# Kernel tuning notes

Hardware: AMD Instinct MI355X
Metric: run time of the kernel (lower is better)

## Reference

```python
import jax, jax.numpy as jnp
import numpy as np

B, T, D_IN, H, NH, R = 32, 1024, 64, 128, 4, 3
HD = H // NH  # 32


def _p(key, shape, scale=0.02):
    return jax.random.normal(key, shape, dtype=jnp.float32) * scale


def setup_inputs() -> dict:
    key = jax.random.key(0)
    ks = jax.random.split(key, 8)
    return {
        "x": jax.random.normal(ks[0], (B, T, D_IN), dtype=jnp.float32),
        "theta_w": _p(ks[1], (H, D_IN)),
        "theta_b": jnp.zeros((H,), jnp.float32),
        "in_proj_w": _p(ks[2], (3 * H, H)),
        "in_proj_b": jnp.zeros((3 * H,), jnp.float32),
        "out_proj_w": _p(ks[3], (H, H)),
        "out_proj_b": jnp.zeros((H,), jnp.float32),
        "ln_g": jnp.ones((H,), jnp.float32),
        "ln_b": jnp.zeros((H,), jnp.float32),
        "w1": _p(ks[4], (H, H)),
        "b1": jnp.zeros((H,), jnp.float32),
        "w2": _p(ks[5], (2, H)),
        "b2": jnp.zeros((2,), jnp.float32),
    }


def _build_adj(t, radius):
    # banded adjacency: adj[i,j] = 1/(1+|i-j|) for |i-j| <= radius, row-normalized
    idx = jnp.arange(t)
    d = jnp.abs(idx[:, None] - idx[None, :])
    adj = jnp.where(d <= radius, 1.0 / (1.0 + d.astype(jnp.float32)), 0.0)
    return adj / jnp.clip(adj.sum(axis=1, keepdims=True), 1e-8)


def reference(x, theta_w, theta_b, in_proj_w, in_proj_b, out_proj_w, out_proj_b,
              ln_g, ln_b, w1, b1, w2, b2):
    h = x @ theta_w.T + theta_b                       # [B,T,H]
    adj = _build_adj(T, R)                            # [T,T]
    g = jnp.einsum('ij,bjh->bih', adj, h)             # banded temporal aggregation

    # torch nn.MultiheadAttention (batch_first, eval -> no dropout)
    qkv = g @ in_proj_w.T + in_proj_b                 # [B,T,3H]
    q, k, v = jnp.split(qkv, 3, axis=-1)
    split_heads = lambda t: t.reshape(B, T, NH, HD).transpose(0, 2, 1, 3)
    q, k, v = split_heads(q), split_heads(k), split_heads(v)
    scores = jnp.einsum('bntd,bnsd->bnts', q, k) / jnp.sqrt(jnp.float32(HD))
    attn = jax.nn.softmax(scores, axis=-1)
    o = jnp.einsum('bnts,bnsd->bntd', attn, v)
    o = o.transpose(0, 2, 1, 3).reshape(B, T, H)
    a = o @ out_proj_w.T + out_proj_b                 # [B,T,H]

    # head on last timestep: LayerNorm -> Linear -> GELU(exact) -> Linear
    last = a[:, -1, :]                                # [B,H]
    mu = last.mean(-1, keepdims=True)
    var = ((last - mu) ** 2).mean(-1, keepdims=True)
    ln = (last - mu) / jnp.sqrt(var + 1e-5) * ln_g + ln_b
    hid = jax.nn.gelu(ln @ w1.T + b1, approximate=False)
    return hid @ w2.T + b2                            # [B,2]
```

## Files before the change

### kernel.cpp

```cpp
#include <hip/hip_runtime.h>
#include <math.h>

#define TT 1024

__global__ __launch_bounds__(256) void k_qr(
    const float* __restrict__ x, const float* __restrict__ theta_w,
    const float* __restrict__ theta_b, const float* __restrict__ ipw,
    const float* __restrict__ ipb, float* __restrict__ r_out) {
  const int b = blockIdx.x;
  const int tid = threadIdx.x;
  __shared__ float s_xs[64];
  __shared__ float s_y[128];
  __shared__ float s_q[128];
  __shared__ float s_z[4][128];
  const float* __restrict__ xb = x + (size_t)b * TT * 64;

  if (tid < 64) {
    float acc = xb[(TT - 1) * 64 + tid]
              + 0.5f        * xb[(TT - 2) * 64 + tid]
              + (1.f / 3.f) * xb[(TT - 3) * 64 + tid]
              + 0.25f       * xb[(TT - 4) * 64 + tid];
    s_xs[tid] = acc * (12.f / 25.f);
  }
  __syncthreads();
  if (tid < 128) {
    const float* tr = theta_w + tid * 64;
    float acc = theta_b[tid];
    for (int d = 0; d < 64; ++d) acc += tr[d] * s_xs[d];
    s_y[tid] = acc;
  }
  __syncthreads();
  {
    const int g = tid >> 4, l = tid & 15;
    for (int pass = 0; pass < 8; ++pass) {
      const int e = pass * 16 + g;
      const float* wr = ipw + e * 128 + l * 8;
      float acc = 0.f;
      #pragma unroll
      for (int u = 0; u < 8; ++u) acc += wr[u] * s_y[l * 8 + u];
      acc += __shfl_xor(acc, 1);
      acc += __shfl_xor(acc, 2);
      acc += __shfl_xor(acc, 4);
      acc += __shfl_xor(acc, 8);
      if (l == 0) s_q[e] = acc + ipb[e];
    }
  }
  __syncthreads();
  for (int rep = 0; rep < 2; ++rep) {
    const int idx = tid + rep * 256;
    const int n = idx >> 7, c = idx & 127;
    const float* qn = &s_q[n * 32];
    float acc = 0.f;
    for (int e = 0; e < 32; ++e) acc += ipw[(128 + n * 32 + e) * 128 + c] * qn[e];
    s_z[n][c] = acc;
  }
  __syncthreads();
  {
    const int n = tid >> 6, d = tid & 63;
    const float* zn = s_z[n];
    float acc = 0.f;
    for (int c = 0; c < 128; ++c) acc += theta_w[c * 64 + d] * zn[c];
    r_out[(b * 4 + n) * 64 + d] = acc * 0.17677669529663687f;
  }
}

__global__ __launch_bounds__(256) void k_t(
    const float* __restrict__ x, const float* __restrict__ r_in,
    float* __restrict__ t_out) {
  const int b = blockIdx.x >> 4;
  const int chunk = blockIdx.x & 15;
  const int tid = threadIdx.x;
  __shared__ __align__(16) float s_r[256];
  s_r[tid] = r_in[b * 256 + tid];
  __syncthreads();
  const int g = tid >> 4, l = tid & 15;
  const float4 r0 = ((const float4*)(s_r +   0))[l];
  const float4 r1 = ((const float4*)(s_r +  64))[l];
  const float4 r2 = ((const float4*)(s_r + 128))[l];
  const float4 r3 = ((const float4*)(s_r + 192))[l];
  const float* __restrict__ xb = x + ((size_t)b * TT + chunk * 64) * 64;
  for (int it = 0; it < 4; ++it) {
    const int jj = it * 16 + g;
    const float4 xv = ((const float4*)(xb + jj * 64))[l];
    float p0 = xv.x * r0.x + xv.y * r0.y + xv.z * r0.z + xv.w * r0.w;
    float p1 = xv.x * r1.x + xv.y * r1.y + xv.z * r1.z + xv.w * r1.w;
    float p2 = xv.x * r2.x + xv.y * r2.y + xv.z * r2.z + xv.w * r2.w;
    float p3 = xv.x * r3.x + xv.y * r3.y + xv.z * r3.z + xv.w * r3.w;
    #pragma unroll
    for (int m = 1; m <= 8; m <<= 1) {
      p0 += __shfl_xor(p0, m);
      p1 += __shfl_xor(p1, m);
      p2 += __shfl_xor(p2, m);
      p3 += __shfl_xor(p3, m);
    }
    if (l == 0) {
      const int j = chunk * 64 + jj;
      t_out[(b * 4 + 0) * TT + j] = p0;
      t_out[(b * 4 + 1) * TT + j] = p1;
      t_out[(b * 4 + 2) * TT + j] = p2;
      t_out[(b * 4 + 3) * TT + j] = p3;
    }
  }
}

__global__ __launch_bounds__(256) void k_sm(float* __restrict__ t_pt) {
  const int bn = blockIdx.x;
  const int tid = threadIdx.x;
  __shared__ __align__(16) float s_t[TT];
  __shared__ float s_p[TT];
  __shared__ float s_red[4];
  ((float4*)s_t)[tid] = ((const float4*)(t_pt + bn * TT))[tid];
  __syncthreads();

  float sc[4], wsv[4];
  float lmax = -1e30f;
  const int s0 = tid * 4;
  for (int k = 0; k < 4; ++k) {
    const int s = s0 + k;
    float acc = 0.f, wsum = 0.f;
    #pragma unroll
    for (int dj = -3; dj <= 3; ++dj) {
      const int j = s + dj;
      if (j >= 0 && j < TT) {
        const float w = 1.f / (1.f + (float)(dj < 0 ? -dj : dj));
        acc += w * s_t[j];
        wsum += w;
      }
    }
    sc[k] = acc / wsum;
    wsv[k] = wsum;
    lmax = fmaxf(lmax, sc[k]);
  }
  #pragma unroll
  for (int m = 32; m >= 1; m >>= 1) lmax = fmaxf(lmax, __shfl_xor(lmax, m));
  if ((tid & 63) == 0) s_red[tid >> 6] = lmax;
  __syncthreads();
  const float bmax = fmaxf(fmaxf(s_red[0], s_red[1]), fmaxf(s_red[2], s_red[3]));
  __syncthreads();
  float lsum = 0.f;
  for (int k = 0; k < 4; ++k) {
    const float e = expf(sc[k] - bmax);
    lsum += e;
    s_p[s0 + k] = e / wsv[k];
  }
  #pragma unroll
  for (int m = 32; m >= 1; m >>= 1) lsum += __shfl_xor(lsum, m);
  if ((tid & 63) == 0) s_red[tid >> 6] = lsum;
  __syncthreads();
  const float inv_denom = 1.f / (s_red[0] + s_red[1] + s_red[2] + s_red[3]);
  for (int k = 0; k < 4; ++k) {
    const int j = s0 + k;
    float acc = 0.f;
    #pragma unroll
    for (int dj = -3; dj <= 3; ++dj) {
      const int s = j + dj;
      if (s >= 0 && s < TT)
        acc += (1.f / (1.f + (float)(dj < 0 ? -dj : dj))) * s_p[s];
    }
    t_pt[bn * TT + j] = acc * inv_denom;
  }
}

__global__ __launch_bounds__(256) void k_u(
    const float* __restrict__ x, const float* __restrict__ pt_in,
    float* __restrict__ up_out) {
  const int b = blockIdx.x >> 4;
  const int chunk = blockIdx.x & 15;
  const int tid = threadIdx.x;
  __shared__ __align__(16) float s_x[64][64];
  __shared__ float s_p[4][64];
  const float* __restrict__ xb = x + ((size_t)b * TT + chunk * 64) * 64;
  #pragma unroll
  for (int it = 0; it < 4; ++it) {
    const int i4 = tid + it * 256;
    ((float4*)&s_x[0][0])[i4] = ((const float4*)xb)[i4];
  }
  {
    const int n = tid >> 6, jj = tid & 63;
    s_p[n][jj] = pt_in[(b * 4 + n) * TT + chunk * 64 + jj];
  }
  __syncthreads();
  const int n = tid >> 6, d = tid & 63;
  float acc = 0.f;
  for (int jj = 0; jj < 64; ++jj) acc += s_p[n][jj] * s_x[jj][d];
  up_out[((b * 16 + chunk) * 4 + n) * 64 + d] = acc;
}

__global__ __launch_bounds__(128) void k_tail(
    const float* __restrict__ up_in, const float* __restrict__ theta_w,
    const float* __restrict__ theta_b, const float* __restrict__ ipw,
    const float* __restrict__ ipb, const float* __restrict__ Wout,
    const float* __restrict__ outb, const float* __restrict__ ln_g,
    const float* __restrict__ ln_b, const float* __restrict__ w1,
    const float* __restrict__ b1, const float* __restrict__ w2,
    const float* __restrict__ b2, float* __restrict__ out) {
  const int b = blockIdx.x;
  const int tid = threadIdx.x;
  __shared__ float s_u[256];
  __shared__ float s_w[4][128];
  __shared__ float s_o[128], s_ln[128], s_hid[128], s_red[2];

  for (int rep = 0; rep < 2; ++rep) {
    const int idx = tid + rep * 128;
    float acc = 0.f;
    for (int c = 0; c < 16; ++c) acc += up_in[(b * 16 + c) * 256 + idx];
    s_u[idx] = acc;
  }
  __syncthreads();
  for (int rep = 0; rep < 4; ++rep) {
    const int idx = tid + rep * 128;
    const int n = idx >> 7, c = idx & 127;
    const float* tr = theta_w + c * 64;
    const float* un = &s_u[n * 64];
    float acc = theta_b[c];
    for (int d = 0; d < 64; ++d) acc += tr[d] * un[d];
    s_w[n][c] = acc;
  }
  __syncthreads();
  {
    const int e = tid, n = e >> 5;
    const float* wr = ipw + (256 + e) * 128;
    const float* wn = s_w[n];
    float acc = ipb[256 + e];
    for (int c = 0; c < 128; ++c) acc += wr[c] * wn[c];
    s_o[e] = acc;
  }
  __syncthreads();
  const int e = tid;
  float a = outb[e];
  {
    const float* wr = Wout + e * 128;
    for (int f = 0; f < 128; ++f) a += wr[f] * s_o[f];
  }
  float sum = a;
  #pragma unroll
  for (int m = 32; m >= 1; m >>= 1) sum += __shfl_xor(sum, m);
  if ((e & 63) == 0) s_red[e >> 6] = sum;
  __syncthreads();
  const float mu = (s_red[0] + s_red[1]) * (1.f / 128.f);
  __syncthreads();
  const float d = a - mu;
  float sq = d * d;
  #pragma unroll
  for (int m = 32; m >= 1; m >>= 1) sq += __shfl_xor(sq, m);
  if ((e & 63) == 0) s_red[e >> 6] = sq;
  __syncthreads();
  const float var = (s_red[0] + s_red[1]) * (1.f / 128.f);
  const float ln = d / sqrtf(var + 1e-5f) * ln_g[e] + ln_b[e];
  s_ln[e] = ln;
  __syncthreads();
  float h = b1[e];
  {
    const float* w1r = w1 + e * 128;
    for (int f = 0; f < 128; ++f) h += w1r[f] * s_ln[f];
  }
  h = 0.5f * h * (1.f + erff(h * 0.70710678118654752f));
  s_hid[e] = h;
  __syncthreads();
  if (e < 2) {
    float acc = b2[e];
    const float* w2r = w2 + e * 128;
    for (int f = 0; f < 128; ++f) acc += w2r[f] * s_hid[f];
    out[b * 2 + e] = acc;
  }
}

extern "C" void kernel_launch(void* const* d_in, const int* in_sizes, int n_in,
                              void* d_out, int out_size, void* d_ws, size_t ws_size,
                              hipStream_t stream) {
  const float* x       = (const float*)d_in[0];
  const float* theta_w = (const float*)d_in[1];
  const float* theta_b = (const float*)d_in[2];
  const float* ipw     = (const float*)d_in[3];
  const float* ipb     = (const float*)d_in[4];
  const float* outw    = (const float*)d_in[5];
  const float* outb    = (const float*)d_in[6];
  const float* ln_g    = (const float*)d_in[7];
  const float* ln_b    = (const float*)d_in[8];
  const float* w1      = (const float*)d_in[9];
  const float* b1      = (const float*)d_in[10];
  const float* w2      = (const float*)d_in[11];
  const float* b2      = (const float*)d_in[12];

  float* ws = (float*)d_ws;
  float* r  = ws;
  float* t  = ws + 8192;
  float* up = ws + 8192 + 131072;

  k_qr  <<< 32, 256, 0, stream>>>(x, theta_w, theta_b, ipw, ipb, r);
  k_t   <<<512, 256, 0, stream>>>(x, r, t);
  k_sm  <<<128, 256, 0, stream>>>(t);
  k_u   <<<512, 256, 0, stream>>>(x, t, up);
  k_tail<<< 32, 128, 0, stream>>>(up, theta_w, theta_b, ipw, ipb, outw, outb,
                                  ln_g, ln_b, w1, b1, w2, b2, (float*)d_out);
}
```

Before: 118.0 us.

## Fuse score, softmax, aggregation and head into one kernel via last-block counter

```diff
diff --git a/kernel.cpp b/kernel.cpp
--- a/kernel.cpp
+++ b/kernel.cpp
@@ -2,11 +2,13 @@
 #include <math.h>
 
 #define TT 1024
+
 
 __global__ __launch_bounds__(256) void k_qr(
     const float* __restrict__ x, const float* __restrict__ theta_w,
     const float* __restrict__ theta_b, const float* __restrict__ ipw,
-    const float* __restrict__ ipb, float* __restrict__ r_out) {
+    const float* __restrict__ ipb, float* __restrict__ r_out,
+    int* __restrict__ cnt) {
   const int b = blockIdx.x;
   const int tid = threadIdx.x;
   __shared__ float s_xs[64];
@@ -15,6 +17,8 @@
   __shared__ float s_z[4][128];
   const float* __restrict__ xb = x + (size_t)b * TT * 64;
 
+  if (tid == 0) cnt[b] = 0;
+
   if (tid < 64) {
     float acc = xb[(TT - 1) * 64 + tid]
               + 0.5f        * xb[(TT - 2) * 64 + tid]
@@ -64,204 +68,210 @@
   }
 }
 
-__global__ __launch_bounds__(256) void k_t(
+__global__ __launch_bounds__(256) void k_main(
     const float* __restrict__ x, const float* __restrict__ r_in,
-    float* __restrict__ t_out) {
+    float* __restrict__ t_ws, int* __restrict__ cnt,
+    const float* __restrict__ theta_w, const float* __restrict__ theta_b,
+    const float* __restrict__ ipw, const float* __restrict__ ipb,
+    const float* __restrict__ Wout, const float* __restrict__ outb,
+    const float* __restrict__ ln_g, const float* __restrict__ ln_b,
+    const float* __restrict__ w1, const float* __restrict__ b1,
+    const float* __restrict__ w2, const float* __restrict__ b2,
+    float* __restrict__ out) {
   const int b = blockIdx.x >> 4;
   const int chunk = blockIdx.x & 15;
   const int tid = threadIdx.x;
+
   __shared__ __align__(16) float s_r[256];
-  s_r[tid] = r_in[b * 256 + tid];
-  __syncthreads();
-  const int g = tid >> 4, l = tid & 15;
-  const float4 r0 = ((const float4*)(s_r +   0))[l];
-  const float4 r1 = ((const float4*)(s_r +  64))[l];
-  const float4 r2 = ((const float4*)(s_r + 128))[l];
-  const float4 r3 = ((const float4*)(s_r + 192))[l];
-  const float* __restrict__ xb = x + ((size_t)b * TT + chunk * 64) * 64;
-  for (int it = 0; it < 4; ++it) {
-    const int jj = it * 16 + g;
-    const float4 xv = ((const float4*)(xb + jj * 64))[l];
-    float p0 = xv.x * r0.x + xv.y * r0.y + xv.z * r0.z + xv.w * r0.w;
-    float p1 = xv.x * r1.x + xv.y * r1.y + xv.z * r1.z + xv.w * r1.w;
-    float p2 = xv.x * r2.x + xv.y * r2.y + xv.z * r2.z + xv.w * r2.w;
-    float p3 = xv.x * r3.x + xv.y * r3.y + xv.z * r3.z + xv.w * r3.w;
-    #pragma unroll
-    for (int m = 1; m <= 8; m <<= 1) {
-      p0 += __shfl_xor(p0, m);
-      p1 += __shfl_xor(p1, m);
-      p2 += __shfl_xor(p2, m);
-      p3 += __shfl_xor(p3, m);
-    }
-    if (l == 0) {
-      const int j = chunk * 64 + jj;
-      t_out[(b * 4 + 0) * TT + j] = p0;
-      t_out[(b * 4 + 1) * TT + j] = p1;
-      t_out[(b * 4 + 2) * TT + j] = p2;
-      t_out[(b * 4 + 3) * TT + j] = p3;
-    }
-  }
-}
-
-__global__ __launch_bounds__(256) void k_sm(float* __restrict__ t_pt) {
-  const int bn = blockIdx.x;
-  const int tid = threadIdx.x;
-  __shared__ __align__(16) float s_t[TT];
-  __shared__ float s_p[TT];
-  __shared__ float s_red[4];
-  ((float4*)s_t)[tid] = ((const float4*)(t_pt + bn * TT))[tid];
-  __syncthreads();
-
-  float sc[4], wsv[4];
-  float lmax = -1e30f;
-  const int s0 = tid * 4;
-  for (int k = 0; k < 4; ++k) {
-    const int s = s0 + k;
-    float acc = 0.f, wsum = 0.f;
-    #pragma unroll
-    for (int dj = -3; dj <= 3; ++dj) {
-      const int j = s + dj;
-      if (j >= 0 && j < TT) {
-        const float w = 1.f / (1.f + (float)(dj < 0 ? -dj : dj));
-        acc += w * s_t[j];
-        wsum += w;
-      }
-    }
-    sc[k] = acc / wsum;
-    wsv[k] = wsum;
-    lmax = fmaxf(lmax, sc[k]);
-  }
-  #pragma unroll
-  for (int m = 32; m >= 1; m >>= 1) lmax = fmaxf(lmax, __shfl_xor(lmax, m));
-  if ((tid & 63) == 0) s_red[tid >> 6] = lmax;
-  __syncthreads();
-  const float bmax = fmaxf(fmaxf(s_red[0], s_red[1]), fmaxf(s_red[2], s_red[3]));
-  __syncthreads();
-  float lsum = 0.f;
-  for (int k = 0; k < 4; ++k) {
-    const float e = expf(sc[k] - bmax);
-    lsum += e;
-    s_p[s0 + k] = e / wsv[k];
-  }
-  #pragma unroll
-  for (int m = 32; m >= 1; m >>= 1) lsum += __shfl_xor(lsum, m);
-  if ((tid & 63) == 0) s_red[tid >> 6] = lsum;
-  __syncthreads();
-  const float inv_denom = 1.f / (s_red[0] + s_red[1] + s_red[2] + s_red[3]);
-  for (int k = 0; k < 4; ++k) {
-    const int j = s0 + k;
-    float acc = 0.f;
-    #pragma unroll
-    for (int dj = -3; dj <= 3; ++dj) {
-      const int s = j + dj;
-      if (s >= 0 && s < TT)
-        acc += (1.f / (1.f + (float)(dj < 0 ? -dj : dj))) * s_p[s];
-    }
-    t_pt[bn * TT + j] = acc * inv_denom;
-  }
-}
-
-__global__ __launch_bounds__(256) void k_u(
-    const float* __restrict__ x, const float* __restrict__ pt_in,
-    float* __restrict__ up_out) {
-  const int b = blockIdx.x >> 4;
-  const int chunk = blockIdx.x & 15;
-  const int tid = threadIdx.x;
-  __shared__ __align__(16) float s_x[64][64];
-  __shared__ float s_p[4][64];
-  const float* __restrict__ xb = x + ((size_t)b * TT + chunk * 64) * 64;
-  #pragma unroll
-  for (int it = 0; it < 4; ++it) {
-    const int i4 = tid + it * 256;
-    ((float4*)&s_x[0][0])[i4] = ((const float4*)xb)[i4];
-  }
-  {
-    const int n = tid >> 6, jj = tid & 63;
-    s_p[n][jj] = pt_in[(b * 4 + n) * TT + chunk * 64 + jj];
-  }
-  __syncthreads();
-  const int n = tid >> 6, d = tid & 63;
-  float acc = 0.f;
-  for (int jj = 0; jj < 64; ++jj) acc += s_p[n][jj] * s_x[jj][d];
-  up_out[((b * 16 + chunk) * 4 + n) * 64 + d] = acc;
-}
-
-__global__ __launch_bounds__(128) void k_tail(
-    const float* __restrict__ up_in, const float* __restrict__ theta_w,
-    const float* __restrict__ theta_b, const float* __restrict__ ipw,
-    const float* __restrict__ ipb, const float* __restrict__ Wout,
-    const float* __restrict__ outb, const float* __restrict__ ln_g,
-    const float* __restrict__ ln_b, const float* __restrict__ w1,
-    const float* __restrict__ b1, const float* __restrict__ w2,
-    const float* __restrict__ b2, float* __restrict__ out) {
-  const int b = blockIdx.x;
-  const int tid = threadIdx.x;
+  __shared__ __align__(16) float s_t[4096];
+  __shared__ __align__(16) float s_p[4096];
+  __shared__ __align__(16) float s_x[4096];
   __shared__ float s_u[256];
   __shared__ float s_w[4][128];
   __shared__ float s_o[128], s_ln[128], s_hid[128], s_red[2];
+  __shared__ int s_flag;
+
+  const float* __restrict__ xb = x + (size_t)b * TT * 64;
+
+  s_r[tid] = r_in[b * 256 + tid];
+  __syncthreads();
+  {
+    const int g = tid >> 4, l = tid & 15;
+    const float4 r0 = ((const float4*)(s_r +   0))[l];
+    const float4 r1 = ((const float4*)(s_r +  64))[l];
+    const float4 r2 = ((const float4*)(s_r + 128))[l];
+    const float4 r3 = ((const float4*)(s_r + 192))[l];
+    const float* __restrict__ xc = xb + chunk * 64 * 64;
+    for (int it = 0; it < 4; ++it) {
+      const int jj = it * 16 + g;
+      const float4 xv = ((const float4*)(xc + jj * 64))[l];
+      float p0 = xv.x * r0.x + xv.y * r0.y + xv.z * r0.z + xv.w * r0.w;
+      float p1 = xv.x * r1.x + xv.y * r1.y + xv.z * r1.z + xv.w * r1.w;
+      float p2 = xv.x * r2.x + xv.y * r2.y + xv.z * r2.z + xv.w * r2.w;
+      float p3 = xv.x * r3.x + xv.y * r3.y + xv.z * r3.z + xv.w * r3.w;
+      #pragma unroll
+      for (int m = 1; m <= 8; m <<= 1) {
+        p0 += __shfl_xor(p0, m);
+        p1 += __shfl_xor(p1, m);
+        p2 += __shfl_xor(p2, m);
+        p3 += __shfl_xor(p3, m);
+      }
+      if (l == 0) {
+        const int j = chunk * 64 + jj;
+        t_ws[(b * 4 + 0) * TT + j] = p0;
+        t_ws[(b * 4 + 1) * TT + j] = p1;
+        t_ws[(b * 4 + 2) * TT + j] = p2;
+        t_ws[(b * 4 + 3) * TT + j] = p3;
+      }
+    }
+  }
+
+  __syncthreads();
+  if (tid == 0) {
+    __threadfence();
+    s_flag = atomicAdd(&cnt[b], 1);
+  }
+  __syncthreads();
+  if (s_flag != 15) return;
+  __threadfence();
+
+  {
+    const float* tb = t_ws + b * 4096;
+    #pragma unroll
+    for (int it = 0; it < 4; ++it)
+      ((float4*)s_t)[tid + it * 256] = ((const float4*)tb)[tid + it * 256];
+  }
+  __syncthreads();
+  const int n = tid >> 6;
+  const int l = tid & 63;
+  {
+    const float* tn = s_t + (n << 10);
+    float* pn = s_p + (n << 10);
+    float sc[16], wsv[16];
+    float lmax = -1e30f;
+    #pragma unroll
+    for (int k = 0; k < 16; ++k) {
+      const int s = (k << 6) + l;
+      float acc = 0.f, wsum = 0.f;
+      #pragma unroll
+      for (int dj = -3; dj <= 3; ++dj) {
+        const int j = s + dj;
+        if (j >= 0 && j < TT) {
+          const float w = 1.f / (1.f + (float)(dj < 0 ? -dj : dj));
+          acc += w * tn[j];
+          wsum += w;
+        }
+      }
+      sc[k] = acc / wsum;
+      wsv[k] = wsum;
+      lmax = fmaxf(lmax, sc[k]);
+    }
+    #pragma unroll
+    for (int m = 32; m >= 1; m >>= 1) lmax = fmaxf(lmax, __shfl_xor(lmax, m));
+    float lsum = 0.f;
+    #pragma unroll
+    for (int k = 0; k < 16; ++k) {
+      const float e = expf(sc[k] - lmax);
+      lsum += e;
+      pn[(k << 6) + l] = e / wsv[k];
+    }
+    #pragma unroll
+    for (int m = 32; m >= 1; m >>= 1) lsum += __shfl_xor(lsum, m);
+    const float invd = 1.f / lsum;
+    __syncthreads();
+    float* ptn = s_t + (n << 10);
+    #pragma unroll
+    for (int k = 0; k < 16; ++k) {
+      const int j = (k << 6) + l;
+      float acc = 0.f;
+      #pragma unroll
+      for (int dj = -3; dj <= 3; ++dj) {
+        const int s = j + dj;
+        if (s >= 0 && s < TT)
+          acc += (1.f / (1.f + (float)(dj < 0 ? -dj : dj))) * pn[s];
+      }
+      ptn[j] = acc * invd;
+    }
+  }
+  __syncthreads();
+
+  {
+    const int d = tid & 63;
+    const float* ptn = s_t + (n << 10);
+    float accu = 0.f;
+    for (int c = 0; c < 16; ++c) {
+      __syncthreads();
+      #pragma unroll
+      for (int it = 0; it < 4; ++it)
+        ((float4*)s_x)[tid + it * 256] =
+            ((const float4*)(xb + (c << 12)))[tid + it * 256];
+      __syncthreads();
+      const float* pc = ptn + (c << 6);
+      #pragma unroll 16
+      for (int jj = 0; jj < 64; ++jj) accu += pc[jj] * s_x[(jj << 6) + d];
+    }
+    s_u[tid] = accu;
+  }
+  __syncthreads();
 
   for (int rep = 0; rep < 2; ++rep) {
-    const int idx = tid + rep * 128;
-    float acc = 0.f;
-    for (int c = 0; c < 16; ++c) acc += up_in[(b * 16 + c) * 256 + idx];
-    s_u[idx] = acc;
-  }
-  __syncthreads();
-  for (int rep = 0; rep < 4; ++rep) {
-    const int idx = tid + rep * 128;
-    const int n = idx >> 7, c = idx & 127;
+    const int idx = tid + rep * 256;
+    const int nn = idx >> 7, c = idx & 127;
     const float* tr = theta_w + c * 64;
-    const float* un = &s_u[n * 64];
+    const float* un = &s_u[nn * 64];
     float acc = theta_b[c];
     for (int d = 0; d < 64; ++d) acc += tr[d] * un[d];
-    s_w[n][c] = acc;
-  }
-  __syncthreads();
-  {
-    const int e = tid, n = e >> 5;
+    s_w[nn][c] = acc;
+  }
+  __syncthreads();
+  if (tid < 128) {
+    const int e = tid, nn = e >> 5;
     const float* wr = ipw + (256 + e) * 128;
-    const float* wn = s_w[n];
     float acc = ipb[256 + e];
-    for (int c = 0; c < 128; ++c) acc += wr[c] * wn[c];
+    for (int c = 0; c < 128; ++c) acc += wr[c] * s_w[nn][c];
     s_o[e] = acc;
   }
   __syncthreads();
-  const int e = tid;
-  float a = outb[e];
-  {
-    const float* wr = Wout + e * 128;
+  float a = 0.f;
+  if (tid < 128) {
+    a = outb[tid];
+    const float* wr = Wout + tid * 128;
     for (int f = 0; f < 128; ++f) a += wr[f] * s_o[f];
   }
   float sum = a;
   #pragma unroll
   for (int m = 32; m >= 1; m >>= 1) sum += __shfl_xor(sum, m);
-  if ((e & 63) == 0) s_red[e >> 6] = sum;
+  if (tid == 0) s_red[0] = sum;
+  if (tid == 64) s_red[1] = sum;
   __syncthreads();
   const float mu = (s_red[0] + s_red[1]) * (1.f / 128.f);
   __syncthreads();
-  const float d = a - mu;
-  float sq = d * d;
+  const float dv = (tid < 128) ? (a - mu) : 0.f;
+  float sq = dv * dv;
   #pragma unroll
   for (int m = 32; m >= 1; m >>= 1) sq += __shfl_xor(sq, m);
-  if ((e & 63) == 0) s_red[e >> 6] = sq;
+  if (tid == 0) s_red[0] = sq;
+  if (tid == 64) s_red[1] = sq;
   __syncthreads();
   const float var = (s_red[0] + s_red[1]) * (1.f / 128.f);
-  const float ln = d / sqrtf(var + 1e-5f) * ln_g[e] + ln_b[e];
-  s_ln[e] = ln;
-  __syncthreads();
-  float h = b1[e];
-  {
-    const float* w1r = w1 + e * 128;
+  if (tid < 128) {
+    const float ln = dv / sqrtf(var + 1e-5f) * ln_g[tid] + ln_b[tid];
+    s_ln[tid] = ln;
+  }
+  __syncthreads();
+  if (tid < 128) {
+    float h = b1[tid];
+    const float* w1r = w1 + tid * 128;
     for (int f = 0; f < 128; ++f) h += w1r[f] * s_ln[f];
-  }
-  h = 0.5f * h * (1.f + erff(h * 0.70710678118654752f));
-  s_hid[e] = h;
-  __syncthreads();
-  if (e < 2) {
-    float acc = b2[e];
-    const float* w2r = w2 + e * 128;
+    h = 0.5f * h * (1.f + erff(h * 0.70710678118654752f));
+    s_hid[tid] = h;
+  }
+  __syncthreads();
+  if (tid < 2) {
+    float acc = b2[tid];
+    const float* w2r = w2 + tid * 128;
     for (int f = 0; f < 128; ++f) acc += w2r[f] * s_hid[f];
-    out[b * 2 + e] = acc;
+    out[b * 2 + tid] = acc;
   }
 }
 
@@ -283,14 +293,12 @@
   const float* b2      = (const float*)d_in[12];
 
   float* ws = (float*)d_ws;
-  float* r  = ws;
-  float* t  = ws + 8192;
-  float* up = ws + 8192 + 131072;
-
-  k_qr  <<< 32, 256, 0, stream>>>(x, theta_w, theta_b, ipw, ipb, r);
-  k_t   <<<512, 256, 0, stream>>>(x, r, t);
-  k_sm  <<<128, 256, 0, stream>>>(t);
-  k_u   <<<512, 256, 0, stream>>>(x, t, up);
-  k_tail<<< 32, 128, 0, stream>>>(up, theta_w, theta_b, ipw, ipb, outw, outb,
-                                  ln_g, ln_b, w1, b1, w2, b2, (float*)d_out);
+  int*   cnt = (int*)d_ws;
+  float* r   = ws + 64;
+  float* t   = ws + 8256;
+
+  k_qr  <<< 32, 256, 0, stream>>>(x, theta_w, theta_b, ipw, ipb, r, cnt);
+  k_main<<<512, 256, 0, stream>>>(x, r, t, cnt, theta_w, theta_b, ipw, ipb,
+                                  outw, outb, ln_g, ln_b, w1, b1, w2, b2,
+                                  (float*)d_out);
 }
```

Result: slower. 160.9 us (+36.3%).
